# Kernel optimization log

Hardware: AMD Instinct MI355X
Metric: run time of the kernel (lower is better)

The kernel has to match this reference:

```python
import jax, jax.numpy as jnp
import numpy as np
from jax import lax

BITWIDTH = 7
EPS = 1e-5


def ti_quant(x):
    """TiFloatToInt8: per-tensor int8 quantization with power-of-2 scale."""
    rng = jnp.max(jnp.abs(x))
    bw = jnp.ceil(jnp.log2(rng))
    exp = bw - BITWIDTH
    q = jnp.clip(jnp.round(x * 2.0 ** (BITWIDTH - bw)), -128.0, 127.0)
    return q, exp


def ti_conv(xv, xe, wv, we, pad):
    """TiConv2d: integer conv (simulated in f32, all values int-valued),
    int32 accumulate, then shift back to 8 bits; exponents add."""
    acc = lax.conv_general_dilated(
        xv, wv, window_strides=(1, 1), padding=[(pad, pad), (pad, pad)],
        dimension_numbers=("NCHW", "OIHW", "NCHW"))
    rng = jnp.max(jnp.abs(acc))
    bw = jnp.ceil(jnp.log2(rng))
    shift = jnp.maximum(bw - BITWIDTH, 0.0)
    q = jnp.clip(jnp.round(acc * 2.0 ** (-shift)), -128.0, 127.0)
    return q, xe + we + shift


def batchnorm(x, gamma, beta):
    # training-mode BN: batch statistics over (N, H, W)
    mean = jnp.mean(x, axis=(0, 2, 3), keepdims=True)
    var = jnp.var(x, axis=(0, 2, 3), keepdims=True)
    g = gamma[None, :, None, None]
    b = beta[None, :, None, None]
    return g * (x - mean) * lax.rsqrt(var + EPS) + b


def setup_inputs() -> dict:
    key = jax.random.key(0)
    k0, k1, k2, k3, k4 = jax.random.split(key, 5)
    B, Cin, Cout, H, W = 32, 128, 256, 56, 56
    x_val = jax.random.randint(k0, (B, Cin, H, W), -128, 128, dtype=jnp.int32)
    x_exp = jnp.zeros((), jnp.float32) - 7.0
    wDW = jnp.round(jnp.clip(jax.random.normal(k1, (Cin, Cin, 3, 3), jnp.float32) * 32.0, -128.0, 127.0))
    wDW_exp = jnp.zeros((), jnp.float32) - 9.0
    wPW = jnp.round(jnp.clip(jax.random.normal(k2, (Cout, Cin, 1, 1), jnp.float32) * 32.0, -128.0, 127.0))
    wPW_exp = jnp.zeros((), jnp.float32) - 9.0
    gamma1 = jnp.ones((Cin,), jnp.float32) + 0.1 * jax.random.normal(k3, (Cin,), jnp.float32)
    beta1 = jnp.zeros((Cin,), jnp.float32)
    gamma2 = jnp.ones((Cout,), jnp.float32) + 0.1 * jax.random.normal(k4, (Cout,), jnp.float32)
    beta2 = jnp.zeros((Cout,), jnp.float32)
    return {"x_val": x_val, "x_exp": x_exp, "wDW": wDW, "wDW_exp": wDW_exp,
            "wPW": wPW, "wPW_exp": wPW_exp, "gamma1": gamma1, "beta1": beta1,
            "gamma2": gamma2, "beta2": beta2}


def reference(x_val, x_exp, wDW, wDW_exp, wPW, wPW_exp, gamma1, beta1, gamma2, beta2):
    xv = x_val.astype(jnp.float32)
    # convDW (3x3, in->in, pad=1)
    q, e = ti_conv(xv, x_exp, wDW, wDW_exp, 1)
    # dequant -> bn1 -> quant
    f = batchnorm(q * 2.0 ** e, gamma1, beta1)
    q, e = ti_quant(f)
    # TiReLU on int values
    q = jnp.maximum(q, 0.0)
    # convPW (1x1, in->out)
    q, e = ti_conv(q, e, wPW, wPW_exp, 0)
    # dequant -> bn2 -> quant -> relu
    f = batchnorm(q * 2.0 ** e, gamma2, beta2)
    q, e = ti_quant(f)
    q = jnp.maximum(q, 0.0)
    return q.astype(jnp.int8), e
```

## Files before the change

### kernel.cpp

```cpp
#include <hip/hip_runtime.h>
#include <cstdint>
#include <cstddef>

#define C1 128
#define C2 256
#define Hh 56
#define Wd 56
#define HW 3136
#define NHW 100352
#define N1 ((size_t)12845056)
#define N2 ((size_t)25690112)
#define XPSZ ((size_t)13778944)
#define NREP 8

typedef int v4i __attribute__((ext_vector_type(4)));
typedef int v16i __attribute__((ext_vector_type(16)));

static constexpr size_t OFF_XP = 0;
static constexpr size_t OFF_Q1 = XPSZ;
static constexpr size_t OFF_Q3 = OFF_Q1 + N1;
static constexpr size_t OFF_WQ1 = OFF_Q3 + N2;
static constexpr size_t OFF_WQ2 = OFF_WQ1 + 147456;
static constexpr size_t OFF_STATS = OFF_WQ2 + 32768;

struct Stats {
  int absmax1, absmax2, tick1, tick2;
  float scale1, e1, s2, e2;
  float scaleq2, e3, sf, ef;
  int sum1[NREP][C1]; unsigned sumsq1[NREP][C1];
  int min1[NREP][C1], max1[NREP][C1];
  float A1[C1], B1c[C1];
  int sum2[NREP][C2]; unsigned sumsq2[NREP][C2];
  int min2[NREP][C2], max2[NREP][C2];
  float A2[C2], B2c[C2];
};

__global__ __launch_bounds__(256) void k_pre(
    const int* __restrict__ x, signed char* __restrict__ xp,
    const float* __restrict__ wDW, signed char* __restrict__ wq1t,
    const float* __restrict__ wPW, signed char* __restrict__ wq2t,
    Stats* st) {
  __shared__ signed char lds[56 * 132];
  int t = threadIdx.x, bid = blockIdx.x;
  if (bid < 1856) {
    int hh = bid % 58, n = bid / 58;
    int* xpw = (int*)(xp + ((size_t)n * 58 + hh) * 7424);
    if (hh == 0 || hh == 57) {
      for (int o = t; o < 1856; o += 256) xpw[o] = 0;
      return;
    }
    int h = hh - 1;
    const int* xb = x + (size_t)n * C1 * HW + h * 56;
    for (int idx = t; idx < 7168; idx += 256) {
      int c = idx / 56, w = idx - c * 56;
      lds[w * 132 + c] = (signed char)xb[(size_t)c * HW + w];
    }
    __syncthreads();
    for (int o = t; o < 1856; o += 256) {
      int kb = o / 232, r = o - kb * 232, ww = r >> 2, cw = r & 3;
      int val = (ww == 0 || ww == 57) ? 0
                : *(const int*)&lds[(ww - 1) * 132 + kb * 16 + cw * 4];
      xpw[o] = val;
    }
    return;
  }
  if (bid < 2432) {
    int idx = (bid - 1856) * 256 + t;
    int co = idx / 1152, r = idx - co * 1152;
    int ci = r / 9, pos = r - ci * 9;
    int k = pos * 128 + ci;
    wq1t[(size_t)(k >> 4) * 2048 + co * 16 + (k & 15)] = (signed char)(int)wDW[idx];
    return;
  }
  if (bid < 2560) {
    int i = (bid - 2432) * 256 + t;
    int co = i >> 7, ci = i & 127;
    wq2t[(size_t)(ci >> 4) * 4096 + co * 16 + (ci & 15)] = (signed char)(int)wPW[i];
    return;
  }
  if (t == 0) { st->absmax1 = 0; st->absmax2 = 0; st->tick1 = 0; st->tick2 = 0; }
  for (int c = t; c < NREP * C1; c += 256) {
    ((int*)st->sum1)[c] = 0; ((unsigned*)st->sumsq1)[c] = 0u;
    ((int*)st->min1)[c] = 127; ((int*)st->max1)[c] = -128;
  }
  for (int c = t; c < NREP * C2; c += 256) {
    ((int*)st->sum2)[c] = 0; ((unsigned*)st->sumsq2)[c] = 0u;
    ((int*)st->min2)[c] = 127; ((int*)st->max2)[c] = -128;
  }
}

__device__ inline v4i ld16_lds(const signed char* p) {
  const int2* q = (const int2*)p;
  int2 lo = q[0], hi = q[1];
  v4i r; r[0] = lo.x; r[1] = lo.y; r[2] = hi.x; r[3] = hi.y;
  return r;
}

__device__ inline float bn_affine_v(int sum, unsigned sumsq, int mn, int mx,
                                    float g, float b, float e_in,
                                    float* Aout, float* Bout) {
  double meanq = (double)sum / (double)NHW;
  double varq = (double)sumsq / (double)NHW - meanq * meanq;
  float se = exp2f(e_in);
  float mean = (float)meanq * se;
  float var = (float)varq * se * se;
  float rsq = 1.0f / sqrtf(var + 1e-5f);
  float Avv = g * se * rsq;
  float Bvv = b - g * mean * rsq;
  *Aout = Avv; *Bout = Bvv;
  return fmaxf(fabsf(Avv * (float)mn + Bvv), fabsf(Avv * (float)mx + Bvv));
}

__device__ inline void conv1_mfma(const signed char* __restrict__ xp,
                                  const signed char* __restrict__ wq1t,
                                  int bx, int t, v16i a1[2][4]) {
  int lane = t & 63, wave = t >> 6;
  int half = lane >> 5, l31 = lane & 31;
  size_t g0 = (size_t)bx * 256;

  const signed char* ab[2];
#pragma unroll
  for (int i = 0; i < 2; ++i) {
    size_t gm = g0 + wave * 64 + i * 32 + l31;
    int n = (int)(gm / HW);
    int p = (int)(gm - (size_t)n * HW);
    int h = p / 56, w = p - h * 56;
    ab[i] = xp + ((size_t)n * 58 + h) * 7424 + w * 16 + half * 928;
  }
  const signed char* bb[4];
#pragma unroll
  for (int j = 0; j < 4; ++j)
    bb[j] = wq1t + (size_t)(j * 32 + l31) * 16 + half * 2048;

#pragma unroll
  for (int i = 0; i < 2; ++i)
#pragma unroll
    for (int j = 0; j < 4; ++j)
#pragma unroll
      for (int r = 0; r < 16; ++r) a1[i][j][r] = 0;

#pragma unroll
  for (int pos = 0; pos < 9; ++pos) {
    int kh = pos / 3, kw = pos - kh * 3;
    const signed char* a0p = ab[0] + kh * 7424 + kw * 16;
    const signed char* a1p = ab[1] + kh * 7424 + kw * 16;
#pragma unroll
    for (int kb = 0; kb < 8; kb += 2) {
      v4i af0 = *(const v4i*)(a0p + kb * 928);
      v4i af1 = *(const v4i*)(a1p + kb * 928);
      v4i bf[4];
#pragma unroll
      for (int j = 0; j < 4; ++j)
        bf[j] = *(const v4i*)(bb[j] + pos * 16384 + kb * 2048);
#pragma unroll
      for (int j = 0; j < 4; ++j) {
        a1[0][j] = __builtin_amdgcn_mfma_i32_32x32x32_i8(af0, bf[j], a1[0][j], 0, 0, 0);
        a1[1][j] = __builtin_amdgcn_mfma_i32_32x32x32_i8(af1, bf[j], a1[1][j], 0, 0, 0);
      }
    }
  }
}

__global__ __launch_bounds__(256, 2) void k_conv1a(
    const signed char* __restrict__ xp, const signed char* __restrict__ wq1t,
    Stats* st) {
  __shared__ int reda[4];
  int t = threadIdx.x, lane = t & 63, wave = t >> 6;
  v16i a1[2][4];
  conv1_mfma(xp, wq1t, blockIdx.x, t, a1);

  int am = 0;
#pragma unroll
  for (int i = 0; i < 2; ++i)
#pragma unroll
    for (int j = 0; j < 4; ++j)
#pragma unroll
      for (int r = 0; r < 16; ++r) am = max(am, abs(a1[i][j][r]));
  for (int off = 32; off; off >>= 1) am = max(am, __shfl_down(am, off, 64));
  if (lane == 0) reda[wave] = am;
  __syncthreads();
  if (t == 0)
    atomicMax(&st->absmax1, max(max(reda[0], reda[1]), max(reda[2], reda[3])));
}

__global__ __launch_bounds__(256, 2) void k_conv1b(
    const signed char* __restrict__ xp, const signed char* __restrict__ wq1t,
    signed char* __restrict__ q1, Stats* st,
    const float* __restrict__ x_exp, const float* __restrict__ wDW_exp,
    const float* __restrict__ gamma1, const float* __restrict__ beta1) {
  __shared__ int qti[256 * 34];
  __shared__ int psum[C1], psq[C1], pmn[C1], pmx[C1];
  __shared__ float redc[2];
  __shared__ int lastf;
  signed char* qt = (signed char*)qti;
  int t = threadIdx.x, lane = t & 63, wave = t >> 6;
  int half = lane >> 5, l31 = lane & 31;
  int rep = blockIdx.x & (NREP - 1);

  v16i a1[2][4];
  conv1_mfma(xp, wq1t, blockIdx.x, t, a1);

  if (t < C1) { psum[t] = 0; psq[t] = 0; pmn[t] = 127; pmx[t] = -128; }
  __syncthreads();

  int v1 = st->absmax1;
  int pw = 31 - __clz(v1 | 1);
  int bw = ((v1 & (v1 - 1)) == 0) ? pw : pw + 1;
  int sh = max(bw - 7, 0);
  float scale1 = exp2f((float)(-sh));
  float e1 = x_exp[0] + wDW_exp[0] + (float)sh;
  if (blockIdx.x == 0 && t == 0) st->e1 = e1;

#pragma unroll
  for (int j = 0; j < 4; ++j) {
    int sj = 0, sqj = 0, mnj = 127, mxj = -128;
    int c = j * 32 + l31;
#pragma unroll
    for (int i = 0; i < 2; ++i)
#pragma unroll
      for (int reg = 0; reg < 16; ++reg) {
        int av = a1[i][j][reg];
        int row = (reg & 3) + 8 * (reg >> 2) + 4 * half;
        int pix = wave * 64 + i * 32 + row;
        float r = rintf((float)av * scale1);
        r = fminf(fmaxf(r, -128.f), 127.f);
        int qi = (int)r;
        qt[pix * 136 + c] = (signed char)qi;
        sj += qi; sqj += qi * qi; mnj = min(mnj, qi); mxj = max(mxj, qi);
      }
    sj += __shfl_down(sj, 32, 64);
    sqj += __shfl_down(sqj, 32, 64);
    mnj = min(mnj, __shfl_down(mnj, 32, 64));
    mxj = max(mxj, __shfl_down(mxj, 32, 64));
    if (half == 0) {
      atomicAdd(&psum[c], sj); atomicAdd(&psq[c], sqj);
      atomicMin(&pmn[c], mnj); atomicMax(&pmx[c], mxj);
    }
  }
  __syncthreads();
  if (t < C1) {
    atomicAdd(&st->sum1[rep][t], psum[t]);
    atomicAdd(&st->sumsq1[rep][t], (unsigned)psq[t]);
    atomicMin(&st->min1[rep][t], pmn[t]);
    atomicMax(&st->max1[rep][t], pmx[t]);
  }
  int* q1w = (int*)(q1 + (size_t)blockIdx.x * 256 * 128);
  for (int idx = t; idx < 8192; idx += 256)
    q1w[idx] = qti[(idx >> 5) * 34 + (idx & 31)];

  __syncthreads();
  if (t == 0) lastf = (atomicAdd(&st->tick1, 1) == 391);
  __syncthreads();
  if (lastf) {
    if (t < C1) {
      int sm = 0; unsigned sq = 0; int mn = 127, mx = -128;
#pragma unroll
      for (int r2 = 0; r2 < NREP; ++r2) {
        sm += atomicAdd(&st->sum1[r2][t], 0);
        sq += atomicAdd(&st->sumsq1[r2][t], 0u);
        mn = min(mn, atomicMin(&st->min1[r2][t], 127));
        mx = max(mx, atomicMax(&st->max1[r2][t], -128));
      }
      float cand = bn_affine_v(sm, sq, mn, mx, gamma1[t], beta1[t], e1,
                               &st->A1[t], &st->B1c[t]);
      for (int off = 32; off; off >>= 1) cand = fmaxf(cand, __shfl_down(cand, off, 64));
      if ((t & 63) == 0) redc[t >> 6] = cand;
    }
    __syncthreads();
    if (t == 0) {
      float rng = fmaxf(redc[0], redc[1]);
      float bwv = ceilf(log2f(rng));
      st->s2 = exp2f(7.0f - bwv);
      st->e2 = bwv - 7.0f;
    }
  }
}

template <int STORE>
__global__ __launch_bounds__(256, 2) void k_conv2t(
    const signed char* __restrict__ q1, const signed char* __restrict__ wq2t,
    signed char* __restrict__ q3, Stats* st, const float* __restrict__ wPW_exp,
    const float* __restrict__ gamma2, const float* __restrict__ beta2,
    float* __restrict__ out) {
  __shared__ __align__(16) signed char wq2s[32768];
  __shared__ int qti[128 * 34];
  __shared__ int psum[C2], psq[C2], pmn[C2], pmx[C2];
  __shared__ int reda[4];
  __shared__ float red2[4];
  __shared__ int lastf;
  signed char* qt = (signed char*)qti;

  int t = threadIdx.x, lane = t & 63, wave = t >> 6;
  int half = lane >> 5, l31 = lane & 31;
  size_t g0 = (size_t)blockIdx.x * 128;
  int rep = blockIdx.x & (NREP - 1);

  v4i wtmp[8];
#pragma unroll
  for (int i = 0; i < 8; ++i)
    wtmp[i] = *(const v4i*)(wq2t + i * 4096 + t * 16);
  const int* q1w = (const int*)(q1 + g0 * 128);
  int qv[16];
#pragma unroll
  for (int k = 0; k < 16; ++k) qv[k] = q1w[k * 256 + t];

  if (STORE) { psum[t] = 0; psq[t] = 0; pmn[t] = 127; pmx[t] = -128; }

  int c4 = t & 31;
  float Av[4], Bv[4];
#pragma unroll
  for (int jj = 0; jj < 4; ++jj) {
    Av[jj] = st->A1[c4 * 4 + jj];
    Bv[jj] = st->B1c[c4 * 4 + jj];
  }
  float s2 = st->s2;

#pragma unroll
  for (int i = 0; i < 8; ++i)
    *(v4i*)(wq2s + i * 4096 + t * 16) = wtmp[i];

#pragma unroll
  for (int k = 0; k < 16; ++k) {
    int v = qv[k];
    int pix = (k * 256 + t) >> 5;
    int outv = 0;
#pragma unroll
    for (int jj = 0; jj < 4; ++jj) {
      int b = (signed char)(v >> (8 * jj));
      float y = Av[jj] * (float)b + Bv[jj];
      float r = rintf(y * s2);
      r = fminf(fmaxf(r, -128.f), 127.f);
      r = fmaxf(r, 0.f);
      outv |= ((int)r & 0xff) << (8 * jj);
    }
    qti[pix * 34 + c4] = outv;
  }
  __syncthreads();

  v16i acc[8];
#pragma unroll
  for (int j = 0; j < 8; ++j)
#pragma unroll
    for (int r = 0; r < 16; ++r) acc[j][r] = 0;

#pragma unroll
  for (int ks = 0; ks < 4; ++ks) {
    v4i af = ld16_lds(&qt[(wave * 32 + l31) * 136 + half * 16 + ks * 32]);
#pragma unroll
    for (int j = 0; j < 8; ++j) {
      v4i bf = *(const v4i*)(wq2s + (size_t)(ks * 2 + half) * 4096 + (j * 32 + l31) * 16);
      acc[j] = __builtin_amdgcn_mfma_i32_32x32x32_i8(af, bf, acc[j], 0, 0, 0);
    }
  }

  if (STORE == 0) {
    int am2 = 0;
#pragma unroll
    for (int j = 0; j < 8; ++j)
#pragma unroll
      for (int r = 0; r < 16; ++r) am2 = max(am2, abs(acc[j][r]));
    for (int off = 32; off; off >>= 1) am2 = max(am2, __shfl_down(am2, off, 64));
    if (lane == 0) reda[wave] = am2;
    __syncthreads();
    if (t == 0)
      atomicMax(&st->absmax2, max(max(reda[0], reda[1]), max(reda[2], reda[3])));
  } else {
    int v2 = st->absmax2;
    int pw = 31 - __clz(v2 | 1);
    int bw = ((v2 & (v2 - 1)) == 0) ? pw : pw + 1;
    int sh2 = max(bw - 7, 0);
    float scale2 = exp2f((float)(-sh2));
    float e3 = st->e2 + wPW_exp[0] + (float)sh2;
    if (blockIdx.x == 0 && t == 0) st->e3 = e3;
    int* q3w = (int*)(q3 + (size_t)blockIdx.x * 32768);
#pragma unroll
    for (int j = 0; j < 8; ++j) {
      int c = j * 32 + l31;
      int sj = 0, sqj = 0, mnj = 127, mxj = -128;
#pragma unroll
      for (int rg = 0; rg < 4; ++rg) {
        int pk = 0;
#pragma unroll
        for (int b = 0; b < 4; ++b) {
          float r = rintf((float)acc[j][4 * rg + b] * scale2);
          r = fminf(fmaxf(r, -128.f), 127.f);
          int qi = (int)r;
          pk |= (qi & 0xff) << (8 * b);
          sj += qi; sqj += qi * qi; mnj = min(mnj, qi); mxj = max(mxj, qi);
        }
        q3w[((wave * 8 + j) * 4 + rg) * 64 + lane] = pk;
      }
      sj += __shfl_down(sj, 32, 64);
      sqj += __shfl_down(sqj, 32, 64);
      mnj = min(mnj, __shfl_down(mnj, 32, 64));
      mxj = max(mxj, __shfl_down(mxj, 32, 64));
      if (half == 0) {
        atomicAdd(&psum[c], sj); atomicAdd(&psq[c], sqj);
        atomicMin(&pmn[c], mnj); atomicMax(&pmx[c], mxj);
      }
    }
    __syncthreads();
    atomicAdd(&st->sum2[rep][t], psum[t]);
    atomicAdd(&st->sumsq2[rep][t], (unsigned)psq[t]);
    atomicMin(&st->min2[rep][t], pmn[t]);
    atomicMax(&st->max2[rep][t], pmx[t]);

    __syncthreads();
    if (t == 0) lastf = (atomicAdd(&st->tick2, 1) == 783);
    __syncthreads();
    if (lastf) {
      int sm = 0; unsigned sq = 0; int mn = 127, mx = -128;
#pragma unroll
      for (int r2 = 0; r2 < NREP; ++r2) {
        sm += atomicAdd(&st->sum2[r2][t], 0);
        sq += atomicAdd(&st->sumsq2[r2][t], 0u);
        mn = min(mn, atomicMin(&st->min2[r2][t], 127));
        mx = max(mx, atomicMax(&st->max2[r2][t], -128));
      }
      float cand = bn_affine_v(sm, sq, mn, mx, gamma2[t], beta2[t], e3,
                               &st->A2[t], &st->B2c[t]);
      for (int off = 32; off; off >>= 1) cand = fmaxf(cand, __shfl_down(cand, off, 64));
      if (lane == 0) red2[wave] = cand;
      __syncthreads();
      if (t == 0) {
        float rng = fmaxf(fmaxf(red2[0], red2[1]), fmaxf(red2[2], red2[3]));
        float bwv = ceilf(log2f(rng));
        st->sf = exp2f(7.0f - bwv);
        st->ef = bwv - 7.0f;
        out[N2] = bwv - 7.0f;
      }
    }
  }
}

__global__ __launch_bounds__(256) void k_out(
    const signed char* __restrict__ q3, const Stats* __restrict__ st,
    float* __restrict__ out) {
  __shared__ int ldsc[256 * 17];
  int t = threadIdx.x, lane = t & 63, wave = t >> 6;
  int bid = blockIdx.x;
  size_t g0 = (size_t)bid * 64;
  int n = (int)(g0 / HW), p0 = (int)(g0 - (size_t)n * HW);
  const int* q3r = (const int*)(q3 + (size_t)(bid >> 1) * 32768) + (bid & 1) * 4096;
#pragma unroll
  for (int k = 0; k < 16; ++k) {
    int i = k * 256 + t;
    int ln = i & 63, rg = (i >> 6) & 3, j = (i >> 8) & 7, wv = (i >> 11) & 1;
    int v = q3r[i];
    int c = j * 32 + (ln & 31);
    int psub = wv * 8 + 2 * rg + (ln >> 5);
    ldsc[c * 17 + psub] = v;
  }
  __syncthreads();
  float sf = st->sf;
  float* ob = out + (size_t)n * C2 * HW + p0 + lane;
#pragma unroll
  for (int cg = 0; cg < 64; ++cg) {
    int c = wave * 64 + ((cg + wave * 16) & 63);
    int vv = ldsc[c * 17 + (lane >> 2)];
    float y = st->A2[c] * (float)((signed char)(vv >> (8 * (lane & 3)))) + st->B2c[c];
    float r = rintf(y * sf);
    r = fminf(fmaxf(r, -128.f), 127.f);
    ob[(size_t)c * HW] = fmaxf(r, 0.f);
  }
}

extern "C" void kernel_launch(void* const* d_in, const int* in_sizes, int n_in,
                              void* d_out, int out_size, void* d_ws, size_t ws_size,
                              hipStream_t stream) {
  const int* x = (const int*)d_in[0];
  const float* x_exp = (const float*)d_in[1];
  const float* wDW = (const float*)d_in[2];
  const float* wDW_exp = (const float*)d_in[3];
  const float* wPW = (const float*)d_in[4];
  const float* wPW_exp = (const float*)d_in[5];
  const float* gamma1 = (const float*)d_in[6];
  const float* beta1 = (const float*)d_in[7];
  const float* gamma2 = (const float*)d_in[8];
  const float* beta2 = (const float*)d_in[9];
  float* out = (float*)d_out;

  char* ws = (char*)d_ws;
  signed char* xp2 = (signed char*)(ws + OFF_XP);
  signed char* q1 = (signed char*)(ws + OFF_Q1);
  signed char* q3 = (signed char*)(ws + OFF_Q3);
  signed char* wq1t = (signed char*)(ws + OFF_WQ1);
  signed char* wq2t = (signed char*)(ws + OFF_WQ2);
  Stats* st = (Stats*)(ws + OFF_STATS);

  hipLaunchKernelGGL(k_pre, dim3(2561), dim3(256), 0, stream,
                     x, xp2, wDW, wq1t, wPW, wq2t, st);
  hipLaunchKernelGGL(k_conv1a, dim3(392), dim3(256), 0, stream,
                     xp2, wq1t, st);
  hipLaunchKernelGGL(k_conv1b, dim3(392), dim3(256), 0, stream,
                     xp2, wq1t, q1, st, x_exp, wDW_exp, gamma1, beta1);
  hipLaunchKernelGGL(HIP_KERNEL_NAME(k_conv2t<0>), dim3(784), dim3(256), 0, stream,
                     q1, wq2t, q3, st, wPW_exp, gamma2, beta2, out);
  hipLaunchKernelGGL(HIP_KERNEL_NAME(k_conv2t<1>), dim3(784), dim3(256), 0, stream,
                     q1, wq2t, q3, st, wPW_exp, gamma2, beta2, out);
  hipLaunchKernelGGL(k_out, dim3(1568), dim3(256), 0, stream, q3, st, out);
}
```

Baseline: 279.2 us.

## Fuse two-pass conv1 into one kernel with grid-wide barrier for absmax

Removes the separate absmax pass over conv1, which recomputed the full 3x3 conv MFMA work. A single kernel now computes the accumulators, publishes the block absmax atomically, and spins on a global tick counter until all 392 blocks arrive, then quantizes from registers. Tick counters are padded onto separate cache lines. This relies on all 392 blocks being co-resident (256 CUs at 2 blocks/CU by launch bounds), otherwise it deadlocks.

```diff
diff --git a/kernel.cpp b/kernel.cpp
--- a/kernel.cpp
+++ b/kernel.cpp
@@ -12,6 +12,7 @@
 #define N2 ((size_t)25690112)
 #define XPSZ ((size_t)13778944)
 #define NREP 8
+#define NB1 392
 
 typedef int v4i __attribute__((ext_vector_type(4)));
 typedef int v16i __attribute__((ext_vector_type(16)));
@@ -24,9 +25,13 @@
 static constexpr size_t OFF_STATS = OFF_WQ2 + 32768;
 
 struct Stats {
-  int absmax1, absmax2, tick1, tick2;
+  int absmax1, absmax2, pad0, pad1;
   float scale1, e1, s2, e2;
   float scaleq2, e3, sf, ef;
+  int padA[20];
+  int tick1, padB[31];
+  int tick2, padC[31];
+  int tick3, padD[31];
   int sum1[NREP][C1]; unsigned sumsq1[NREP][C1];
   int min1[NREP][C1], max1[NREP][C1];
   float A1[C1], B1c[C1];
@@ -78,7 +83,10 @@
     wq2t[(size_t)(ci >> 4) * 4096 + co * 16 + (ci & 15)] = (signed char)(int)wPW[i];
     return;
   }
-  if (t == 0) { st->absmax1 = 0; st->absmax2 = 0; st->tick1 = 0; st->tick2 = 0; }
+  if (t == 0) {
+    st->absmax1 = 0; st->absmax2 = 0;
+    st->tick1 = 0; st->tick2 = 0; st->tick3 = 0;
+  }
   for (int c = t; c < NREP * C1; c += 256) {
     ((int*)st->sum1)[c] = 0; ((unsigned*)st->sumsq1)[c] = 0u;
     ((int*)st->min1)[c] = 127; ((int*)st->max1)[c] = -128;
@@ -161,33 +169,13 @@
   }
 }
 
-__global__ __launch_bounds__(256, 2) void k_conv1a(
-    const signed char* __restrict__ xp, const signed char* __restrict__ wq1t,
-    Stats* st) {
-  __shared__ int reda[4];
-  int t = threadIdx.x, lane = t & 63, wave = t >> 6;
-  v16i a1[2][4];
-  conv1_mfma(xp, wq1t, blockIdx.x, t, a1);
-
-  int am = 0;
-#pragma unroll
-  for (int i = 0; i < 2; ++i)
-#pragma unroll
-    for (int j = 0; j < 4; ++j)
-#pragma unroll
-      for (int r = 0; r < 16; ++r) am = max(am, abs(a1[i][j][r]));
-  for (int off = 32; off; off >>= 1) am = max(am, __shfl_down(am, off, 64));
-  if (lane == 0) reda[wave] = am;
-  __syncthreads();
-  if (t == 0)
-    atomicMax(&st->absmax1, max(max(reda[0], reda[1]), max(reda[2], reda[3])));
-}
-
-__global__ __launch_bounds__(256, 2) void k_conv1b(
+__global__ __launch_bounds__(256, 2) void k_conv1f(
     const signed char* __restrict__ xp, const signed char* __restrict__ wq1t,
     signed char* __restrict__ q1, Stats* st,
     const float* __restrict__ x_exp, const float* __restrict__ wDW_exp,
     const float* __restrict__ gamma1, const float* __restrict__ beta1) {
+  __shared__ int reda[4];
+  __shared__ int vbro;
   __shared__ int qti[256 * 34];
   __shared__ int psum[C1], psq[C1], pmn[C1], pmx[C1];
   __shared__ float redc[2];
@@ -200,10 +188,30 @@
   v16i a1[2][4];
   conv1_mfma(xp, wq1t, blockIdx.x, t, a1);
 
+  int am = 0;
+#pragma unroll
+  for (int i = 0; i < 2; ++i)
+#pragma unroll
+    for (int j = 0; j < 4; ++j)
+#pragma unroll
+      for (int r = 0; r < 16; ++r) am = max(am, abs(a1[i][j][r]));
+  for (int off = 32; off; off >>= 1) am = max(am, __shfl_down(am, off, 64));
+  if (lane == 0) reda[wave] = am;
   if (t < C1) { psum[t] = 0; psq[t] = 0; pmn[t] = 127; pmx[t] = -128; }
   __syncthreads();
-
-  int v1 = st->absmax1;
+  if (t == 0)
+    atomicMax(&st->absmax1, max(max(reda[0], reda[1]), max(reda[2], reda[3])));
+  __syncthreads();
+
+  if (t == 0) {
+    atomicAdd(&st->tick1, 1);
+    while (atomicAdd(&st->tick1, 0) < NB1)
+      __builtin_amdgcn_s_sleep(8);
+    vbro = atomicAdd(&st->absmax1, 0);
+  }
+  __syncthreads();
+
+  int v1 = vbro;
   int pw = 31 - __clz(v1 | 1);
   int bw = ((v1 & (v1 - 1)) == 0) ? pw : pw + 1;
   int sh = max(bw - 7, 0);
@@ -249,7 +257,7 @@
     q1w[idx] = qti[(idx >> 5) * 34 + (idx & 31)];
 
   __syncthreads();
-  if (t == 0) lastf = (atomicAdd(&st->tick1, 1) == 391);
+  if (t == 0) lastf = (atomicAdd(&st->tick3, 1) == NB1 - 1);
   __syncthreads();
   if (lastf) {
     if (t < C1) {
@@ -490,9 +498,7 @@
 
   hipLaunchKernelGGL(k_pre, dim3(2561), dim3(256), 0, stream,
                      x, xp2, wDW, wq1t, wPW, wq2t, st);
-  hipLaunchKernelGGL(k_conv1a, dim3(392), dim3(256), 0, stream,
-                     xp2, wq1t, st);
-  hipLaunchKernelGGL(k_conv1b, dim3(392), dim3(256), 0, stream,
+  hipLaunchKernelGGL(k_conv1f, dim3(NB1), dim3(256), 0, stream,
                      xp2, wq1t, q1, st, x_exp, wDW_exp, gamma1, beta1);
   hipLaunchKernelGGL(HIP_KERNEL_NAME(k_conv2t<0>), dim3(784), dim3(256), 0, stream,
                      q1, wq2t, q3, st, wPW_exp, gamma2, beta2, out);
```

Measured after the change: 262.8 us. -5.9%, faster.
